# Performance work log

Hardware: AMD Instinct MI355X
Metric: run time of the kernel (lower is better)

## Reference

```python
import jax, jax.numpy as jnp
import numpy as np

# Loihi CUBA LIF neuron constants (netParams['neuron'])
V_TH_MANT = 80.0
THETA = V_TH_MANT * 64.0          # threshold in voltage units (vThMant << 6)
I_DECAY = 1024.0
V_DECAY = 128.0
REF_DELAY = 1.0
DECAY_U = 1.0 - I_DECAY / 4096.0  # current decay per step
DECAY_V = 1.0 - V_DECAY / 4096.0  # voltage decay per step
TAU_RHO = 1.0
SCALE_RHO = 1.0
POOL_W = 1.1 * V_TH_MANT          # SLAYER pool weight: one input spike -> 1.1*theta drive


@jax.custom_vjp
def spike_fn(v):
    # Heaviside spike with SLAYER surrogate gradient
    return (v >= THETA).astype(v.dtype)

def _spike_fwd(v):
    return spike_fn(v), v

def _spike_bwd(v, g):
    sur = (SCALE_RHO / THETA) * jnp.exp(-jnp.abs(v - THETA) / (TAU_RHO * THETA))
    return (g * sur,)

spike_fn.defvjp(_spike_fwd, _spike_bwd)


def spike_loihi(x):
    """Loihi LIF recurrence over last (time) axis. x: [..., T] weighted spikes."""
    shp = x.shape
    xt = jnp.moveaxis(x.reshape(-1, shp[-1]), -1, 0)  # [T, N]
    z = jnp.zeros(xt.shape[1], x.dtype)
    def step(carry, x_t):
        u, v, ref = carry
        u = u * DECAY_U + x_t * 64.0                  # current state (input scaled by 2^6)
        active = (ref <= 0).astype(x.dtype)
        v = (v * DECAY_V + u) * active                # voltage, clamped in refractory period
        s = spike_fn(v)
        ref = jnp.where(s > 0, REF_DELAY, jnp.maximum(ref - 1.0, 0.0))
        v = v * (1.0 - s)                             # reset on spike
        return (u, v, ref), s
    _, spikes = jax.lax.scan(step, (z, z, z), xt)
    return jnp.moveaxis(spikes, 0, -1).reshape(shp)


def delay_shift(x, d=1):
    # shift spikes forward in time by d steps (zero-pad at t=0)
    return jnp.pad(x, [(0, 0)] * (x.ndim - 1) + [(d, 0)])[..., :x.shape[-1]]


def conv2d_t(x, w):
    # x: [B,C,H,W,T], w: [O,I,k,k]; 2D 'SAME' conv applied independently per timestep
    B, C, H, W, T = x.shape
    xm = jnp.moveaxis(x, -1, 1).reshape(B * T, C, H, W)
    y = jax.lax.conv_general_dilated(xm, w, (1, 1), 'SAME',
                                     dimension_numbers=('NCHW', 'OIHW', 'NCHW'))
    O = w.shape[0]
    return jnp.moveaxis(y.reshape(B, T, O, H, W), 1, -1)


def sum_pool(x, k):
    # SLAYER pool = sum over kxk window * fixed weight (per timestep)
    y = jax.lax.reduce_window(x, 0.0, jax.lax.add,
                              (1, 1, k, k, 1), (1, 1, k, k, 1), 'VALID')
    return y * POOL_W


def setup_inputs() -> dict:
    key = jax.random.key(0)
    ks = jax.random.split(key, 5)
    B, T = 8, 128
    x = (jax.random.uniform(ks[0], (B, 2, 128, 128, T)) < 0.1).astype(jnp.float32)
    w1 = jax.random.normal(ks[1], (16, 2, 5, 5), jnp.float32) * 10.0 * 0.2   # weightScale=10
    w2 = jax.random.normal(ks[2], (32, 16, 3, 3), jnp.float32) * 50.0 * 0.2  # weightScale=50
    wf1 = jax.random.normal(ks[3], (512, 2048), jnp.float32) * 100.0 * 0.02  # dense default scale
    wf2 = jax.random.normal(ks[4], (11, 512), jnp.float32) * 100.0 * 0.02
    return {"x": x, "w1": w1, "w2": w2, "wf1": wf1, "wf2": wf2}


def reference(x, w1, w2, wf1, wf2):
    s = spike_loihi(sum_pool(x, 4))            # [B,2,32,32,T]
    s = delay_shift(s)
    s = spike_loihi(conv2d_t(s, w1))           # [B,16,32,32,T]
    s = delay_shift(s)
    s = spike_loihi(sum_pool(s, 2))            # [B,16,16,16,T]
    s = delay_shift(s)
    s = spike_loihi(conv2d_t(s, w2))           # [B,32,16,16,T]
    s = delay_shift(s)
    s = spike_loihi(sum_pool(s, 2))            # [B,32,8,8,T]
    B, T = s.shape[0], s.shape[-1]
    s = s.reshape(B, -1, T)                    # [B,2048,T]
    s = delay_shift(s)
    s = spike_loihi(jnp.einsum('bft,of->bot', s, wf1))  # [B,512,T]
    s = delay_shift(s)
    s = spike_loihi(jnp.einsum('bft,of->bot', s, wf2))  # [B,11,T]
    s = delay_shift(s)
    return s[:, :, None, None, :]              # [B,11,1,1,T]
```

## Files before the change

kernel.cpp:

```cpp
#include <hip/hip_runtime.h>

#define TT 128

#define DECAY_U 0.75f
#define DECAY_V 0.96875f
#define THETA   5120.0f
#define POOLW   88.0f

__device__ __forceinline__ void lif_step(float xt, float& u, float& v, int& refc, float& s) {
    u = __fadd_rn(__fmul_rn(u, DECAY_U), __fmul_rn(xt, 64.0f));
    float vn = __fadd_rn(__fmul_rn(v, DECAY_V), u);
    v = refc ? 0.0f : vn;
    s = (v >= THETA) ? 1.0f : 0.0f;
    if (s > 0.f) { refc = 1; v = 0.f; }
    else         { refc = refc > 0 ? refc - 1 : 0; }
}

__device__ __forceinline__ void lif_seq_lds(float* col, int stride) {
    float u = 0.f, v = 0.f;
    int refc = 0;
    #pragma unroll 16
    for (int t = 0; t < TT; ++t) {
        float s;
        lif_step(col[t * stride], u, v, refc, s);
        col[t * stride] = s;
    }
}

__global__ void wtrans_k(const float* __restrict__ w1, const float* __restrict__ w2,
                         float* __restrict__ wTg1, float* __restrict__ wTg2) {
    int i = blockIdx.x * 256 + threadIdx.x;
    if (i < 800) {
        int oc = i & 15, ck = i >> 4;
        wTg1[ck*16 + oc] = w1[oc*50 + ck];
    }
    if (i < 4608) {
        int oc = i & 31, ck = i >> 5;
        wTg2[ck*32 + oc] = w2[oc*144 + ck];
    }
}

__global__ void pool1_lif_k(const float* __restrict__ x, float* __restrict__ s1) {
    __shared__ float sb[TT][3];
    int t = threadIdx.x & 127, pos = threadIdx.x >> 7;
    int n = blockIdx.x * 2 + pos;
    int px = n & 31, py = (n >> 5) & 31, c = (n >> 10) & 1, b = n >> 11;
    const float* base = x + (size_t)((((b*2 + c)*128 + py*4)*128) + px*4) * 128 + t;
    float s = 0.f;
    #pragma unroll
    for (int dy = 0; dy < 4; ++dy)
        #pragma unroll
        for (int dx = 0; dx < 4; ++dx)
            s += base[(dy*128 + dx) * 128];
    sb[t][pos] = s * POOLW;
    __syncthreads();
    if (threadIdx.x < 2) lif_seq_lds(&sb[0][threadIdx.x], 3);
    __syncthreads();
    s1[(size_t)n * TT + t] = sb[t][pos];
}

__global__ void pack1_k(const float* __restrict__ s1, unsigned char* __restrict__ pk1) {
    int id = blockIdx.x * 256 + threadIdx.x;
    int t = id & 127;
    int pos = id >> 7;
    int b = pos >> 10, rem = pos & 1023;
    const float* p0 = s1 + (size_t)(b*2) * 131072 + rem * 128 + t;
    unsigned int v = (p0[0] > 0.5f ? 1u : 0u) | (p0[131072] > 0.5f ? 2u : 0u);
    pk1[id] = (unsigned char)v;
}

__global__ void pack2_k(const float* __restrict__ s3, unsigned short* __restrict__ pk3) {
    int id = blockIdx.x * 256 + threadIdx.x;
    int t = id & 127;
    int pos = id >> 7;
    int b = pos >> 8, rem = pos & 255;
    const float* p0 = s3 + (size_t)(b*16) * 32768 + rem * 128 + t;
    unsigned int v = 0;
    #pragma unroll
    for (int c = 0; c < 16; ++c)
        v |= (p0[(size_t)c * 32768] > 0.5f ? 1u : 0u) << c;
    pk3[id] = (unsigned short)v;
}

__global__ __launch_bounds__(256) void conv1_lif_k(const unsigned char* __restrict__ pk1,
                                                   const float* __restrict__ wTg1,
                                                   float* __restrict__ s2) {
    __shared__ float sb[TT][33];
    int id = blockIdx.x * 256 + threadIdx.x;
    int t = id & 127, pos = threadIdx.x >> 7;
    int n = id >> 7;
    int px = n & 31, py = (n >> 5) & 31, b = n >> 10;
    int tsrc = t > 0 ? t - 1 : 0;
    const unsigned char* pp = pk1 + (size_t)b * 131072 + tsrc;
    unsigned int pkv[25];
    #pragma unroll
    for (int ky = 0; ky < 5; ++ky) {
        int iy = py + ky - 2;
        #pragma unroll
        for (int kx = 0; kx < 5; ++kx) {
            int ix = px + kx - 2;
            bool valid = ((unsigned)iy < 32u) && ((unsigned)ix < 32u) && (t > 0);
            int iyc = valid ? iy : 0, ixc = valid ? ix : 0;
            unsigned int v = pp[(iyc*32 + ixc) * 128];
            pkv[ky*5 + kx] = valid ? v : 0u;
        }
    }
    float acc[16];
    #pragma unroll
    for (int k = 0; k < 16; ++k) acc[k] = 0.f;
    #pragma unroll
    for (int tap = 0; tap < 25; ++tap) {
        unsigned int p = pkv[tap];
        float x0 = (float)(p & 1u);
        float x1 = (float)((p >> 1) & 1u);
        const float4* wv0 = (const float4*)&wTg1[tap * 16];
        const float4* wv1 = (const float4*)&wTg1[(25 + tap) * 16];
        #pragma unroll
        for (int j = 0; j < 4; ++j) {
            float4 w = wv0[j];
            acc[j*4+0] = fmaf(w.x, x0, acc[j*4+0]);
            acc[j*4+1] = fmaf(w.y, x0, acc[j*4+1]);
            acc[j*4+2] = fmaf(w.z, x0, acc[j*4+2]);
            acc[j*4+3] = fmaf(w.w, x0, acc[j*4+3]);
        }
        #pragma unroll
        for (int j = 0; j < 4; ++j) {
            float4 w = wv1[j];
            acc[j*4+0] = fmaf(w.x, x1, acc[j*4+0]);
            acc[j*4+1] = fmaf(w.y, x1, acc[j*4+1]);
            acc[j*4+2] = fmaf(w.z, x1, acc[j*4+2]);
            acc[j*4+3] = fmaf(w.w, x1, acc[j*4+3]);
        }
    }
    #pragma unroll
    for (int oc = 0; oc < 16; ++oc) sb[t][oc*2 + pos] = acc[oc];
    __syncthreads();
    if (threadIdx.x < 32) lif_seq_lds(&sb[0][threadIdx.x], 33);
    __syncthreads();
    size_t obase = (((size_t)(b*16) * 32 + py) * 32 + px) * 128 + t;
    #pragma unroll
    for (int oc = 0; oc < 16; ++oc)
        s2[obase + (size_t)oc * 131072] = sb[t][oc*2 + pos];
}

__global__ void pool2_lif_k(const float* __restrict__ s2, float* __restrict__ s3) {
    __shared__ float sb[TT][3];
    int t = threadIdx.x & 127, pos = threadIdx.x >> 7;
    int n = blockIdx.x * 2 + pos;
    int px = n & 15, py = (n >> 4) & 15, c = (n >> 8) & 15, b = n >> 12;
    float acc = 0.f;
    if (t > 0) {
        const float* ip = s2 + (size_t)(((b*16 + c)*32 + py*2)*32 + px*2) * 128 + (t - 1);
        acc = (ip[0] + ip[128] + ip[32*128] + ip[33*128]) * POOLW;
    }
    sb[t][pos] = acc;
    __syncthreads();
    if (threadIdx.x < 2) lif_seq_lds(&sb[0][threadIdx.x], 3);
    __syncthreads();
    s3[(size_t)n * TT + t] = sb[t][pos];
}

__global__ __launch_bounds__(256) void conv2_lif_k(const unsigned short* __restrict__ pk3,
                                                   const float* __restrict__ wTg2,
                                                   float* __restrict__ s4) {
    __shared__ float sb[TT][65];
    int id = blockIdx.x * 256 + threadIdx.x;
    int t = id & 127, pos = threadIdx.x >> 7;
    int n = id >> 7;
    int px = n & 15, py = (n >> 4) & 15, b = n >> 8;
    int tsrc = t > 0 ? t - 1 : 0;
    const unsigned short* pp = pk3 + (size_t)b * 32768 + tsrc;
    unsigned int pkv[9];
    #pragma unroll
    for (int ky = 0; ky < 3; ++ky) {
        int iy = py + ky - 1;
        #pragma unroll
        for (int kx = 0; kx < 3; ++kx) {
            int ix = px + kx - 1;
            bool valid = ((unsigned)iy < 16u) && ((unsigned)ix < 16u) && (t > 0);
            int iyc = valid ? iy : 0, ixc = valid ? ix : 0;
            unsigned int v = pp[(iyc*16 + ixc) * 128];
            pkv[ky*3 + kx] = valid ? v : 0u;
        }
    }
    float acc[32];
    #pragma unroll
    for (int k = 0; k < 32; ++k) acc[k] = 0.f;
    #pragma unroll
    for (int tap = 0; tap < 9; ++tap) {
        unsigned int p = pkv[tap];
        #pragma unroll
        for (int c = 0; c < 16; ++c) {
            float xc = (float)((p >> c) & 1u);
            const float4* wv = (const float4*)&wTg2[(c*9 + tap) * 32];
            #pragma unroll
            for (int j = 0; j < 8; ++j) {
                float4 w = wv[j];
                acc[j*4+0] = fmaf(w.x, xc, acc[j*4+0]);
                acc[j*4+1] = fmaf(w.y, xc, acc[j*4+1]);
                acc[j*4+2] = fmaf(w.z, xc, acc[j*4+2]);
                acc[j*4+3] = fmaf(w.w, xc, acc[j*4+3]);
            }
        }
    }
    #pragma unroll
    for (int oc = 0; oc < 32; ++oc) sb[t][oc*2 + pos] = acc[oc];
    __syncthreads();
    if (threadIdx.x < 64) lif_seq_lds(&sb[0][threadIdx.x], 65);
    __syncthreads();
    size_t obase = (((size_t)(b*32) * 16 + py) * 16 + px) * 128 + t;
    #pragma unroll
    for (int oc = 0; oc < 32; ++oc)
        s4[obase + (size_t)oc * 32768] = sb[t][oc*2 + pos];
}

__global__ void pool3_lif_k(const float* __restrict__ s4, float* __restrict__ s5) {
    __shared__ float sb[TT][3];
    int t = threadIdx.x & 127, pos = threadIdx.x >> 7;
    int n = blockIdx.x * 2 + pos;
    int px = n & 7, py = (n >> 3) & 7, c = (n >> 6) & 31, b = n >> 11;
    float acc = 0.f;
    if (t > 0) {
        const float* ip = s4 + (size_t)(((b*32 + c)*16 + py*2)*16 + px*2) * 128 + (t - 1);
        acc = (ip[0] + ip[128] + ip[16*128] + ip[17*128]) * POOLW;
    }
    sb[t][pos] = acc;
    __syncthreads();
    if (threadIdx.x < 2) lif_seq_lds(&sb[0][threadIdx.x], 3);
    __syncthreads();
    s5[(size_t)n * TT + t] = sb[t][pos];
}

__global__ __launch_bounds__(256) void fc1_gemm_k(const float* __restrict__ s5,
                                                  const float* __restrict__ wf1,
                                                  float* __restrict__ part) {
    __shared__ float WT[64][68];
    __shared__ float ST[64][68];
    int bid = blockIdx.x;
    int kc = bid & 7;
    int ot = (bid >> 3) & 7;
    int tt = (bid >> 6) & 1;
    int b  = bid >> 7;
    int tid = threadIdx.x;
    int oo = tid >> 4;
    int to = tid & 15;

    const float* wbase = wf1 + (size_t)(ot*64) * 2048 + kc*256;
    const float* sbase = s5 + (size_t)b * 262144 + (size_t)(kc*256) * 128;

    float acc[4][4];
    #pragma unroll
    for (int i = 0; i < 4; ++i)
        #pragma unroll
        for (int j = 0; j < 4; ++j) acc[i][j] = 0.f;

    for (int ks = 0; ks < 4; ++ks) {
        __syncthreads();
        #pragma unroll
        for (int i = 0; i < 16; ++i) {
            int e = tid + 256*i;
            int o = e >> 6, f = e & 63;
            WT[f][o] = wbase[(size_t)o * 2048 + ks*64 + f];
        }
        #pragma unroll
        for (int i = 0; i < 16; ++i) {
            int e = tid + 256*i;
            int f = e >> 6, tl = e & 63;
            int tsrc = tt*64 + tl - 1;
            ST[f][tl] = (tsrc < 0) ? 0.f : sbase[(size_t)f * 128 + ks*64*128 + tsrc];
        }
        __syncthreads();
        #pragma unroll 4
        for (int k = 0; k < 64; ++k) {
            float4 a = *(const float4*)&WT[k][oo*4];
            float4 s = *(const float4*)&ST[k][to*4];
            acc[0][0] = fmaf(a.x, s.x, acc[0][0]);
            acc[0][1] = fmaf(a.x, s.y, acc[0][1]);
            acc[0][2] = fmaf(a.x, s.z, acc[0][2]);
            acc[0][3] = fmaf(a.x, s.w, acc[0][3]);
            acc[1][0] = fmaf(a.y, s.x, acc[1][0]);
            acc[1][1] = fmaf(a.y, s.y, acc[1][1]);
            acc[1][2] = fmaf(a.y, s.z, acc[1][2]);
            acc[1][3] = fmaf(a.y, s.w, acc[1][3]);
            acc[2][0] = fmaf(a.z, s.x, acc[2][0]);
            acc[2][1] = fmaf(a.z, s.y, acc[2][1]);
            acc[2][2] = fmaf(a.z, s.z, acc[2][2]);
            acc[2][3] = fmaf(a.z, s.w, acc[2][3]);
            acc[3][0] = fmaf(a.w, s.x, acc[3][0]);
            acc[3][1] = fmaf(a.w, s.y, acc[3][1]);
            acc[3][2] = fmaf(a.w, s.z, acc[3][2]);
            acc[3][3] = fmaf(a.w, s.w, acc[3][3]);
        }
    }
    float* pb = part + (size_t)kc * 524288 + (size_t)b * 65536
              + (size_t)(ot*64 + oo*4) * 128 + tt*64 + to*4;
    #pragma unroll
    for (int i = 0; i < 4; ++i)
        #pragma unroll
        for (int j = 0; j < 4; ++j)
            pb[(size_t)i * 128 + j] = acc[i][j];
}

__global__ void fc1_reduce_lif_k(const float* __restrict__ part, float* __restrict__ s6) {
    __shared__ float sb[TT][3];
    int t = threadIdx.x & 127, pos = threadIdx.x >> 7;
    int n = blockIdx.x * 2 + pos;
    float s = 0.f;
    #pragma unroll
    for (int kc = 0; kc < 8; ++kc)
        s += part[(size_t)kc * 524288 + (size_t)n * 128 + t];
    sb[t][pos] = s;
    __syncthreads();
    if (threadIdx.x < 2) lif_seq_lds(&sb[0][threadIdx.x], 3);
    __syncthreads();
    s6[(size_t)n * TT + t] = sb[t][pos];
}

__global__ void fc2_lif_k(const float* __restrict__ s6, const float* __restrict__ wf2,
                          float* __restrict__ out) {
    __shared__ float sb[TT];
    int t = threadIdx.x;
    int o = blockIdx.x % 11, b = blockIdx.x / 11;
    float acc = 0.f;
    if (t > 0) {
        const float* sp = s6 + (size_t)b * 65536 + (t - 1);
        const float* wp = wf2 + o * 512;
        for (int f = 0; f < 512; f += 4) {
            float4 w = *(const float4*)&wp[f];
            acc = fmaf(w.x, sp[(size_t)f * 128], acc);
            acc = fmaf(w.y, sp[(size_t)(f+1) * 128], acc);
            acc = fmaf(w.z, sp[(size_t)(f+2) * 128], acc);
            acc = fmaf(w.w, sp[(size_t)(f+3) * 128], acc);
        }
    }
    sb[t] = acc;
    __syncthreads();
    if (t == 0) lif_seq_lds(sb, 1);
    __syncthreads();
    float* q = out + (size_t)(b*11 + o) * TT;
    if (t == 0) q[0] = 0.f;
    if (t < TT - 1) q[t + 1] = sb[t];
}

extern "C" void kernel_launch(void* const* d_in, const int* in_sizes, int n_in,
                              void* d_out, int out_size, void* d_ws, size_t ws_size,
                              hipStream_t stream) {
    const float* x   = (const float*)d_in[0];
    const float* w1  = (const float*)d_in[1];
    const float* w2  = (const float*)d_in[2];
    const float* wf1 = (const float*)d_in[3];
    const float* wf2 = (const float*)d_in[4];
    float* out = (float*)d_out;

    float* ws = (float*)d_ws;
    float* A    = ws;
    float* B    = ws + 4194304;
    float* PART = B + 1048576;
    float* D4   = ws + 4194304 + 16777216;
    float* WT1  = D4 + 8388608;
    float* WT2  = WT1 + 800;
    unsigned char*  PK1 = (unsigned char*)(WT2 + 4608);
    unsigned short* PK3 = (unsigned short*)(PK1 + 1048576);

    wtrans_k<<<dim3(18), 256, 0, stream>>>(w1, w2, WT1, WT2);
    pool1_lif_k<<<dim3(8192), 256, 0, stream>>>(x, A);
    pack1_k<<<dim3(4096), 256, 0, stream>>>(A, PK1);
    conv1_lif_k<<<dim3(4096), 256, 0, stream>>>(PK1, WT1, B);
    pool2_lif_k<<<dim3(16384), 256, 0, stream>>>(B, A);
    pack2_k<<<dim3(1024), 256, 0, stream>>>(A, PK3);
    conv2_lif_k<<<dim3(1024), 256, 0, stream>>>(PK3, WT2, D4);
    pool3_lif_k<<<dim3(8192), 256, 0, stream>>>(D4, A);
    fc1_gemm_k      <<<dim3(1024), 256, 0, stream>>>(A, wf1, PART);
    fc1_reduce_lif_k<<<dim3(2048), 256, 0, stream>>>(PART, B);
    fc2_lif_k<<<dim3(88), 128, 0, stream>>>(B, wf2, out);
}
```

Measured before the change: 248.6 us.

## Register-tile conv kernels over four timesteps and split output channels across threads

Conv1 and conv2 now have each thread compute four consecutive timesteps for an 8-output-channel group, rather than one timestep for all channels. Each weight float4 load is then reused across four timesteps, cutting redundant weight fetches. Conv1 processes four pixels per block, so it launches half as many blocks and uses a larger shared LIF buffer. The trade-off is more input byte loads per thread, a different register footprint, and a changed LDS write pattern that could cause bank conflicts.

After: 263.4 us. +5.9%, slower.

```diff
diff --git a/kernel.cpp b/kernel.cpp
--- a/kernel.cpp
+++ b/kernel.cpp
@@ -85,62 +85,89 @@
 __global__ __launch_bounds__(256) void conv1_lif_k(const unsigned char* __restrict__ pk1,
                                                    const float* __restrict__ wTg1,
                                                    float* __restrict__ s2) {
-    __shared__ float sb[TT][33];
-    int id = blockIdx.x * 256 + threadIdx.x;
-    int t = id & 127, pos = threadIdx.x >> 7;
-    int n = id >> 7;
+    __shared__ float sb[TT][65];
+    int tid = threadIdx.x;
+    int t4  = tid & 31;
+    int pos = (tid >> 5) & 3;
+    int ocg = tid >> 7;
+    int n = blockIdx.x * 4 + pos;
     int px = n & 31, py = (n >> 5) & 31, b = n >> 10;
-    int tsrc = t > 0 ? t - 1 : 0;
-    const unsigned char* pp = pk1 + (size_t)b * 131072 + tsrc;
-    unsigned int pkv[25];
+    const unsigned char* pp = pk1 + (size_t)b * 131072;
+
+    float acc[4][8];
+    #pragma unroll
+    for (int i = 0; i < 4; ++i)
+        #pragma unroll
+        for (int k = 0; k < 8; ++k) acc[i][k] = 0.f;
+
     #pragma unroll
     for (int ky = 0; ky < 5; ++ky) {
         int iy = py + ky - 2;
+        unsigned int row[5][4];
         #pragma unroll
         for (int kx = 0; kx < 5; ++kx) {
             int ix = px + kx - 2;
-            bool valid = ((unsigned)iy < 32u) && ((unsigned)ix < 32u) && (t > 0);
-            int iyc = valid ? iy : 0, ixc = valid ? ix : 0;
-            unsigned int v = pp[(iyc*32 + ixc) * 128];
-            pkv[ky*5 + kx] = valid ? v : 0u;
-        }
-    }
-    float acc[16];
-    #pragma unroll
-    for (int k = 0; k < 16; ++k) acc[k] = 0.f;
-    #pragma unroll
-    for (int tap = 0; tap < 25; ++tap) {
-        unsigned int p = pkv[tap];
-        float x0 = (float)(p & 1u);
-        float x1 = (float)((p >> 1) & 1u);
-        const float4* wv0 = (const float4*)&wTg1[tap * 16];
-        const float4* wv1 = (const float4*)&wTg1[(25 + tap) * 16];
-        #pragma unroll
-        for (int j = 0; j < 4; ++j) {
-            float4 w = wv0[j];
-            acc[j*4+0] = fmaf(w.x, x0, acc[j*4+0]);
-            acc[j*4+1] = fmaf(w.y, x0, acc[j*4+1]);
-            acc[j*4+2] = fmaf(w.z, x0, acc[j*4+2]);
-            acc[j*4+3] = fmaf(w.w, x0, acc[j*4+3]);
-        }
-        #pragma unroll
-        for (int j = 0; j < 4; ++j) {
-            float4 w = wv1[j];
-            acc[j*4+0] = fmaf(w.x, x1, acc[j*4+0]);
-            acc[j*4+1] = fmaf(w.y, x1, acc[j*4+1]);
-            acc[j*4+2] = fmaf(w.z, x1, acc[j*4+2]);
-            acc[j*4+3] = fmaf(w.w, x1, acc[j*4+3]);
-        }
-    }
-    #pragma unroll
-    for (int oc = 0; oc < 16; ++oc) sb[t][oc*2 + pos] = acc[oc];
-    __syncthreads();
-    if (threadIdx.x < 32) lif_seq_lds(&sb[0][threadIdx.x], 33);
-    __syncthreads();
-    size_t obase = (((size_t)(b*16) * 32 + py) * 32 + px) * 128 + t;
-    #pragma unroll
-    for (int oc = 0; oc < 16; ++oc)
-        s2[obase + (size_t)oc * 131072] = sb[t][oc*2 + pos];
+            bool vs = ((unsigned)iy < 32u) && ((unsigned)ix < 32u);
+            int iyc = vs ? iy : 0, ixc = vs ? ix : 0;
+            const unsigned char* q = pp + (iyc*32 + ixc) * 128;
+            #pragma unroll
+            for (int i = 0; i < 4; ++i) {
+                int t = t4*4 + i;
+                bool v = vs && (t > 0);
+                unsigned int w = q[v ? t-1 : 0];
+                row[kx][i] = v ? w : 0u;
+            }
+        }
+        #pragma unroll
+        for (int kx = 0; kx < 5; ++kx) {
+            const float4* wv0 = (const float4*)&wTg1[(ky*5 + kx) * 16 + ocg*8];
+            const float4* wv1 = (const float4*)&wTg1[(25 + ky*5 + kx) * 16 + ocg*8];
+            float4 a0 = wv0[0], a1 = wv0[1];
+            float4 c0 = wv1[0], c1 = wv1[1];
+            #pragma unroll
+            for (int i = 0; i < 4; ++i) {
+                float x0 = (float)(row[kx][i] & 1u);
+                float x1 = (float)((row[kx][i] >> 1) & 1u);
+                acc[i][0] = fmaf(a0.x, x0, acc[i][0]);
+                acc[i][1] = fmaf(a0.y, x0, acc[i][1]);
+                acc[i][2] = fmaf(a0.z, x0, acc[i][2]);
+                acc[i][3] = fmaf(a0.w, x0, acc[i][3]);
+                acc[i][4] = fmaf(a1.x, x0, acc[i][4]);
+                acc[i][5] = fmaf(a1.y, x0, acc[i][5]);
+                acc[i][6] = fmaf(a1.z, x0, acc[i][6]);
+                acc[i][7] = fmaf(a1.w, x0, acc[i][7]);
+                acc[i][0] = fmaf(c0.x, x1, acc[i][0]);
+                acc[i][1] = fmaf(c0.y, x1, acc[i][1]);
+                acc[i][2] = fmaf(c0.z, x1, acc[i][2]);
+                acc[i][3] = fmaf(c0.w, x1, acc[i][3]);
+                acc[i][4] = fmaf(c1.x, x1, acc[i][4]);
+                acc[i][5] = fmaf(c1.y, x1, acc[i][5]);
+                acc[i][6] = fmaf(c1.z, x1, acc[i][6]);
+                acc[i][7] = fmaf(c1.w, x1, acc[i][7]);
+            }
+        }
+    }
+    #pragma unroll
+    for (int i = 0; i < 4; ++i) {
+        int t = t4*4 + i;
+        #pragma unroll
+        for (int k = 0; k < 8; ++k)
+            sb[t][(ocg*8 + k)*4 + pos] = acc[i][k];
+    }
+    __syncthreads();
+    if (tid < 64) lif_seq_lds(&sb[0][tid], 65);
+    __syncthreads();
+    int t = tid & 127, pq = tid >> 7;
+    #pragma unroll
+    for (int j = 0; j < 2; ++j) {
+        int pos2 = pq*2 + j;
+        int n2 = blockIdx.x * 4 + pos2;
+        int px2 = n2 & 31, py2 = (n2 >> 5) & 31;
+        size_t obase = (((size_t)(b*16) * 32 + py2) * 32 + px2) * 128 + t;
+        #pragma unroll
+        for (int oc = 0; oc < 16; ++oc)
+            s2[obase + (size_t)oc * 131072] = sb[t][oc*4 + pos2];
+    }
 }
 
 __global__ void pool2_lif_k(const float* __restrict__ s2, float* __restrict__ s3) {
@@ -164,54 +191,77 @@
                                                    const float* __restrict__ wTg2,
                                                    float* __restrict__ s4) {
     __shared__ float sb[TT][65];
-    int id = blockIdx.x * 256 + threadIdx.x;
-    int t = id & 127, pos = threadIdx.x >> 7;
-    int n = id >> 7;
+    int tid = threadIdx.x;
+    int t4  = tid & 31;
+    int pos = (tid >> 5) & 1;
+    int ocg = tid >> 6;
+    int n = blockIdx.x * 2 + pos;
     int px = n & 15, py = (n >> 4) & 15, b = n >> 8;
-    int tsrc = t > 0 ? t - 1 : 0;
-    const unsigned short* pp = pk3 + (size_t)b * 32768 + tsrc;
-    unsigned int pkv[9];
+    const unsigned short* pp = pk3 + (size_t)b * 32768;
+
+    unsigned int pkv[9][4];
     #pragma unroll
     for (int ky = 0; ky < 3; ++ky) {
         int iy = py + ky - 1;
         #pragma unroll
         for (int kx = 0; kx < 3; ++kx) {
             int ix = px + kx - 1;
-            bool valid = ((unsigned)iy < 16u) && ((unsigned)ix < 16u) && (t > 0);
-            int iyc = valid ? iy : 0, ixc = valid ? ix : 0;
-            unsigned int v = pp[(iyc*16 + ixc) * 128];
-            pkv[ky*3 + kx] = valid ? v : 0u;
-        }
-    }
-    float acc[32];
-    #pragma unroll
-    for (int k = 0; k < 32; ++k) acc[k] = 0.f;
-    #pragma unroll
-    for (int tap = 0; tap < 9; ++tap) {
-        unsigned int p = pkv[tap];
-        #pragma unroll
-        for (int c = 0; c < 16; ++c) {
-            float xc = (float)((p >> c) & 1u);
-            const float4* wv = (const float4*)&wTg2[(c*9 + tap) * 32];
+            bool vs = ((unsigned)iy < 16u) && ((unsigned)ix < 16u);
+            int iyc = vs ? iy : 0, ixc = vs ? ix : 0;
+            const unsigned short* q = pp + (iyc*16 + ixc) * 128;
             #pragma unroll
-            for (int j = 0; j < 8; ++j) {
-                float4 w = wv[j];
-                acc[j*4+0] = fmaf(w.x, xc, acc[j*4+0]);
-                acc[j*4+1] = fmaf(w.y, xc, acc[j*4+1]);
-                acc[j*4+2] = fmaf(w.z, xc, acc[j*4+2]);
-                acc[j*4+3] = fmaf(w.w, xc, acc[j*4+3]);
+            for (int i = 0; i < 4; ++i) {
+                int t = t4*4 + i;
+                bool v = vs && (t > 0);
+                unsigned int w = q[v ? t-1 : 0];
+                pkv[ky*3 + kx][i] = v ? w : 0u;
             }
         }
     }
-    #pragma unroll
-    for (int oc = 0; oc < 32; ++oc) sb[t][oc*2 + pos] = acc[oc];
-    __syncthreads();
-    if (threadIdx.x < 64) lif_seq_lds(&sb[0][threadIdx.x], 65);
-    __syncthreads();
-    size_t obase = (((size_t)(b*32) * 16 + py) * 16 + px) * 128 + t;
+
+    float acc[4][8];
+    #pragma unroll
+    for (int i = 0; i < 4; ++i)
+        #pragma unroll
+        for (int k = 0; k < 8; ++k) acc[i][k] = 0.f;
+
+    #pragma unroll
+    for (int c = 0; c < 16; ++c) {
+        #pragma unroll
+        for (int tap = 0; tap < 9; ++tap) {
+            const float4* wv = (const float4*)&wTg2[(c*9 + tap) * 32 + ocg*8];
+            float4 w0 = wv[0], w1 = wv[1];
+            #pragma unroll
+            for (int i = 0; i < 4; ++i) {
+                float xc = (float)((pkv[tap][i] >> c) & 1u);
+                acc[i][0] = fmaf(w0.x, xc, acc[i][0]);
+                acc[i][1] = fmaf(w0.y, xc, acc[i][1]);
+                acc[i][2] = fmaf(w0.z, xc, acc[i][2]);
+                acc[i][3] = fmaf(w0.w, xc, acc[i][3]);
+                acc[i][4] = fmaf(w1.x, xc, acc[i][4]);
+                acc[i][5] = fmaf(w1.y, xc, acc[i][5]);
+                acc[i][6] = fmaf(w1.z, xc, acc[i][6]);
+                acc[i][7] = fmaf(w1.w, xc, acc[i][7]);
+            }
+        }
+    }
+    #pragma unroll
+    for (int i = 0; i < 4; ++i) {
+        int t = t4*4 + i;
+        #pragma unroll
+        for (int k = 0; k < 8; ++k)
+            sb[t][(ocg*8 + k)*2 + pos] = acc[i][k];
+    }
+    __syncthreads();
+    if (tid < 64) lif_seq_lds(&sb[0][tid], 65);
+    __syncthreads();
+    int t = tid & 127, p2 = tid >> 7;
+    int n2 = blockIdx.x * 2 + p2;
+    int px2 = n2 & 15, py2 = (n2 >> 4) & 15;
+    size_t obase = (((size_t)(b*32) * 16 + py2) * 16 + px2) * 128 + t;
     #pragma unroll
     for (int oc = 0; oc < 32; ++oc)
-        s4[obase + (size_t)oc * 32768] = sb[t][oc*2 + pos];
+        s4[obase + (size_t)oc * 32768] = sb[t][oc*2 + p2];
 }
 
 __global__ void pool3_lif_k(const float* __restrict__ s4, float* __restrict__ s5) {
@@ -365,7 +415,7 @@
     wtrans_k<<<dim3(18), 256, 0, stream>>>(w1, w2, WT1, WT2);
     pool1_lif_k<<<dim3(8192), 256, 0, stream>>>(x, A);
     pack1_k<<<dim3(4096), 256, 0, stream>>>(A, PK1);
-    conv1_lif_k<<<dim3(4096), 256, 0, stream>>>(PK1, WT1, B);
+    conv1_lif_k<<<dim3(2048), 256, 0, stream>>>(PK1, WT1, B);
     pool2_lif_k<<<dim3(16384), 256, 0, stream>>>(B, A);
     pack2_k<<<dim3(1024), 256, 0, stream>>>(A, PK3);
     conv2_lif_k<<<dim3(1024), 256, 0, stream>>>(PK3, WT2, D4);
```
